# Performance work log

Measured on AMD Instinct MI355X. Metric: run time of the kernel, lower is better.

The kernel has to match this reference:

```python
import jax, jax.numpy as jnp
import numpy as np

E = 16        # num_experts
K = 2         # num_experts_per_tok
D = 1024      # dim
H = 2816      # moe_intermediate_size
S = 4096      # sequence_length (flattened tokens)


def setup_inputs() -> dict:
    key = jax.random.key(0)
    k0, k1, k2, k3, k4 = jax.random.split(key, 5)
    # gate: nn.Linear(dim, E) default init ~ U(-1/sqrt(D), 1/sqrt(D))
    gb = 1.0 / np.sqrt(D)
    gate_w = jax.random.uniform(k0, (E, D), minval=-gb, maxval=gb, dtype=jnp.float32)
    # MoeFusedLinear init: U(-sqrt(15/in), sqrt(15/in)), weight shape [E, out, in]
    b_d = np.sqrt(15.0 / D)
    b_h = np.sqrt(15.0 / H)
    w_gate = jax.random.uniform(k1, (E, H, D), minval=-b_d, maxval=b_d, dtype=jnp.float32)
    w_up = jax.random.uniform(k2, (E, H, D), minval=-b_d, maxval=b_d, dtype=jnp.float32)
    w_down = jax.random.uniform(k3, (E, D, H), minval=-b_h, maxval=b_h, dtype=jnp.float32)
    hidden_states = jax.random.normal(k4, (S, D), dtype=jnp.float32)
    return {"hidden_states": hidden_states, "gate_w": gate_w,
            "w_gate": w_gate, "w_up": w_up, "w_down": w_down}


def _grouped_mm(x_bf16, w, group_sizes):
    # emulate torch._grouped_mm: bf16 inputs, weight [E, out, in] -> rhs [E, in, out]
    rhs = jnp.swapaxes(w, 1, 2).astype(jnp.bfloat16)
    out = jax.lax.ragged_dot(x_bf16, rhs, group_sizes)
    return out.astype(jnp.float32)  # .to(input.dtype), input is fp32


def reference(hidden_states, gate_w, w_gate, w_up, w_down):
    # --- router (fp32) ---
    logits = hidden_states.astype(jnp.float32) @ gate_w.T              # [S, E]
    probs = jax.nn.softmax(logits, axis=-1)                            # fp32
    top_w, top_i = jax.lax.top_k(probs, K)                             # [S, K]
    rw = top_w / jnp.sum(top_w, axis=-1, keepdims=True)                # norm_topk_prob
    rw = rw.astype(hidden_states.dtype)
    # --- dispatch: replicate tokens K times, stable-sort by expert ---
    flat_e = top_i.reshape(-1)                                         # [S*K]
    sort_idx = jnp.argsort(flat_e, stable=True)
    inv_sort_idx = jnp.argsort(sort_idx)
    x_rep = jnp.repeat(hidden_states, K, axis=0)                       # [S*K, D]
    xs = x_rep[sort_idx].astype(jnp.bfloat16)
    group_sizes = jnp.bincount(flat_e, length=E).astype(jnp.int32)     # histc
    # --- grouped expert MLP (SwiGLU) ---
    g = _grouped_mm(xs, w_gate, group_sizes)                           # [S*K, H] fp32
    u = _grouped_mm(xs, w_up, group_sizes)
    h = (jax.nn.silu(g) * u).astype(jnp.bfloat16)
    y = _grouped_mm(h, w_down, group_sizes)                            # [S*K, D] fp32
    # --- combine ---
    y = y[inv_sort_idx].reshape(S, K, D)
    out = jnp.einsum('sko,sk->so', y, rw)                              # [S, D]
    return out, logits, top_i
```

## Files before the change

### kernel.cpp

```cpp
#include <hip/hip_runtime.h>

#define S_ 4096
#define E_ 16
#define K_ 2
#define D_ 1024
#define H_ 2816
#define MAXT 80
#define MP_ (MAXT * 128)

#define ME_CNT   0
#define ME_FILL  16
#define ME_POFF  32
#define ME_NT    48
#define ME_TE    64
#define ME_TR    (64 + MAXT)

#define WS_META   0
#define WS_SLOT   4096
#define WS_RW     36864
#define WS_TOPI   69632
#define WS_XS     (1u << 20)
#define WS_H      (WS_XS + (size_t)MP_ * D_ * 4)

typedef float floatx4 __attribute__((ext_vector_type(4)));
typedef __bf16 bf16x8 __attribute__((ext_vector_type(8)));

__device__ __forceinline__ unsigned short f2bf(float f) {
  unsigned u = __float_as_uint(f);
  u += 0x7fffu + ((u >> 16) & 1u);
  return (unsigned short)(u >> 16);
}
__device__ __forceinline__ unsigned pack2(float a, float b) {
  return (unsigned)f2bf(a) | ((unsigned)f2bf(b) << 16);
}

__global__ __launch_bounds__(256) void router_k(
    const float* __restrict__ x, const float* __restrict__ gw,
    float* __restrict__ logits_out, float* __restrict__ topi_out,
    float* __restrict__ rw, int* __restrict__ topi, int* __restrict__ meta)
{
  int s = blockIdx.x;
  int t = threadIdx.x;
  __shared__ float xl[D_];
  __shared__ float red[E_][16];
  __shared__ float lg[E_];
  for (int d = t; d < D_; d += 256) xl[d] = x[(size_t)s * D_ + d];
  __syncthreads();
  int e = t >> 4, i = t & 15;
  const float* g = gw + e * D_;
  float p = 0.f;
  for (int j = 0; j < 64; ++j) p += xl[i + 16 * j] * g[i + 16 * j];
  red[e][i] = p;
  __syncthreads();
  if (t < E_) {
    float sm = 0.f;
    for (int j = 0; j < 16; ++j) sm += red[t][j];
    lg[t] = sm;
    logits_out[(size_t)s * E_ + t] = sm;
  }
  __syncthreads();
  if (t == 0) {
    float mx = lg[0];
    for (int j = 1; j < E_; ++j) mx = fmaxf(mx, lg[j]);
    float pr[E_];
    for (int j = 0; j < E_; ++j) pr[j] = expf(lg[j] - mx);
    int i0 = 0; float b0 = pr[0];
    for (int j = 1; j < E_; ++j) if (pr[j] > b0) { b0 = pr[j]; i0 = j; }
    int i1 = -1; float b1 = -1.f;
    for (int j = 0; j < E_; ++j) if (j != i0 && pr[j] > b1) { b1 = pr[j]; i1 = j; }
    float w0 = b0 / (b0 + b1), w1 = b1 / (b0 + b1);
    topi_out[(size_t)s * K_ + 0] = (float)i0;
    topi_out[(size_t)s * K_ + 1] = (float)i1;
    rw[s * K_ + 0] = w0; rw[s * K_ + 1] = w1;
    topi[s * K_ + 0] = i0; topi[s * K_ + 1] = i1;
    atomicAdd(&meta[ME_CNT + i0], 1);
    atomicAdd(&meta[ME_CNT + i1], 1);
  }
}

__global__ void scan_k(int* __restrict__ meta) {
  if (threadIdx.x == 0 && blockIdx.x == 0) {
    int off = 0, nt = 0;
    for (int e = 0; e < E_; ++e) {
      meta[ME_POFF + e] = off;
      int c = meta[ME_CNT + e];
      int tiles = (c + 127) >> 7;
      for (int i = 0; i < tiles; ++i) { meta[ME_TE + nt] = e; meta[ME_TR + nt] = off + i * 128; ++nt; }
      off += tiles << 7;
    }
    meta[ME_NT] = nt;
  }
}

__global__ __launch_bounds__(256) void scatter_k(
    const int* __restrict__ topi, int* __restrict__ meta, int* __restrict__ slot_of)
{
  int idx = blockIdx.x * 256 + threadIdx.x;
  if (idx >= S_ * K_) return;
  int e = topi[idx];
  int pos = meta[ME_POFF + e] + atomicAdd(&meta[ME_FILL + e], 1);
  slot_of[idx] = pos;
}

__global__ __launch_bounds__(256) void gather_k(
    const float* __restrict__ x, const int* __restrict__ slot_of,
    unsigned short* __restrict__ xs)
{
  int idx = blockIdx.x;
  int s = idx >> 1;
  int pos = slot_of[idx];
  int t = threadIdx.x;
  float4 v = ((const float4*)(x + (size_t)s * D_))[t];
  ((uint2*)(xs + (size_t)pos * D_))[t] = make_uint2(pack2(v.x, v.y), pack2(v.z, v.w));
}

__global__ __launch_bounds__(256) void gemm1_k(
    const unsigned short* __restrict__ xs,
    const float* __restrict__ wg, const float* __restrict__ wu,
    unsigned short* __restrict__ h, const int* __restrict__ meta)
{
  int tile = blockIdx.x;
  if (tile >= meta[ME_NT]) return;
  int ntile = blockIdx.y;
  int e = meta[ME_TE + tile];
  int row0 = meta[ME_TR + tile];

  __shared__ uint4 As4[512];
  __shared__ uint4 Bg4[512];
  __shared__ uint4 Bu4[512];
  const unsigned short* As = (const unsigned short*)As4;
  const unsigned short* Bg = (const unsigned short*)Bg4;
  const unsigned short* Bu = (const unsigned short*)Bu4;

  int t = threadIdx.x;
  int lane = t & 63, w = t >> 6;
  int wm = w >> 1, wn = w & 1;

  const unsigned short* ap = xs + (size_t)row0 * D_;
  const float* wgp = wg + ((size_t)e * H_ + ntile * 128) * D_;
  const float* wup = wu + ((size_t)e * H_ + ntile * 128) * D_;

  floatx4 zero4 = {0.f, 0.f, 0.f, 0.f};
  floatx4 accg[4][4], accu[4][4];
  for (int a = 0; a < 4; ++a) for (int b = 0; b < 4; ++b) { accg[a][b] = zero4; accu[a][b] = zero4; }

  int bn = t >> 1, bkh = t & 1;

  for (int k0 = 0; k0 < D_; k0 += 32) {
    __syncthreads();
    {
      int c = t;
      As4[c] = *(const uint4*)(ap + (size_t)(c >> 2) * D_ + k0 + (c & 3) * 8);
      c = t + 256;
      As4[c] = *(const uint4*)(ap + (size_t)(c >> 2) * D_ + k0 + (c & 3) * 8);
    }
    {
      const float4* srcg = (const float4*)(wgp + (size_t)bn * D_ + k0 + bkh * 16);
      const float4* srcu = (const float4*)(wup + (size_t)bn * D_ + k0 + bkh * 16);
      float4 g0 = srcg[0], g1 = srcg[1], g2 = srcg[2], g3 = srcg[3];
      float4 u0 = srcu[0], u1 = srcu[1], u2 = srcu[2], u3 = srcu[3];
      int base = bn * 4 + bkh * 2;
      Bg4[base]     = make_uint4(pack2(g0.x, g0.y), pack2(g0.z, g0.w), pack2(g1.x, g1.y), pack2(g1.z, g1.w));
      Bg4[base + 1] = make_uint4(pack2(g2.x, g2.y), pack2(g2.z, g2.w), pack2(g3.x, g3.y), pack2(g3.z, g3.w));
      Bu4[base]     = make_uint4(pack2(u0.x, u0.y), pack2(u0.z, u0.w), pack2(u1.x, u1.y), pack2(u1.z, u1.w));
      Bu4[base + 1] = make_uint4(pack2(u2.x, u2.y), pack2(u2.z, u2.w), pack2(u3.x, u3.y), pack2(u3.z, u3.w));
    }
    __syncthreads();
    int mrow = lane & 15;
    int kq = (lane >> 4) * 8;
    bf16x8 af[4], bg[4], bu[4];
    for (int mi = 0; mi < 4; ++mi)
      af[mi] = *(const bf16x8*)(As + (wm * 64 + mi * 16 + mrow) * 32 + kq);
    for (int ni = 0; ni < 4; ++ni) {
      int r = (wn * 64 + ni * 16 + mrow) * 32 + kq;
      bg[ni] = *(const bf16x8*)(Bg + r);
      bu[ni] = *(const bf16x8*)(Bu + r);
    }
    for (int mi = 0; mi < 4; ++mi)
      for (int ni = 0; ni < 4; ++ni) {
        accg[mi][ni] = __builtin_amdgcn_mfma_f32_16x16x32_bf16(af[mi], bg[ni], accg[mi][ni], 0, 0, 0);
        accu[mi][ni] = __builtin_amdgcn_mfma_f32_16x16x32_bf16(af[mi], bu[ni], accu[mi][ni], 0, 0, 0);
      }
  }
  int colb = ntile * 128 + wn * 64;
  int rquad = (lane >> 4) * 4;
  for (int mi = 0; mi < 4; ++mi)
    for (int ni = 0; ni < 4; ++ni)
      for (int r = 0; r < 4; ++r) {
        int row = row0 + wm * 64 + mi * 16 + rquad + r;
        int col = colb + ni * 16 + (lane & 15);
        float gv = accg[mi][ni][r], uv = accu[mi][ni][r];
        float sv = gv / (1.f + expf(-gv));
        h[(size_t)row * H_ + col] = f2bf(sv * uv);
      }
}

__global__ __launch_bounds__(256) void gemm2_k(
    const unsigned short* __restrict__ hbuf,
    const float* __restrict__ wd,
    float* __restrict__ y, const int* __restrict__ meta)
{
  int tile = blockIdx.x;
  if (tile >= meta[ME_NT]) return;
  int ntile = blockIdx.y;
  int e = meta[ME_TE + tile];
  int row0 = meta[ME_TR + tile];

  __shared__ uint4 As4[512];
  __shared__ uint4 Bd4[512];
  const unsigned short* As = (const unsigned short*)As4;
  const unsigned short* Bd = (const unsigned short*)Bd4;

  int t = threadIdx.x;
  int lane = t & 63, w = t >> 6;
  int wm = w >> 1, wn = w & 1;

  const unsigned short* ap = hbuf + (size_t)row0 * H_;
  const float* wdp = wd + ((size_t)e * D_ + ntile * 128) * H_;

  floatx4 zero4 = {0.f, 0.f, 0.f, 0.f};
  floatx4 acc[4][4];
  for (int a = 0; a < 4; ++a) for (int b = 0; b < 4; ++b) acc[a][b] = zero4;

  int bn = t >> 1, bkh = t & 1;

  for (int k0 = 0; k0 < H_; k0 += 32) {
    __syncthreads();
    {
      int c = t;
      As4[c] = *(const uint4*)(ap + (size_t)(c >> 2) * H_ + k0 + (c & 3) * 8);
      c = t + 256;
      As4[c] = *(const uint4*)(ap + (size_t)(c >> 2) * H_ + k0 + (c & 3) * 8);
    }
    {
      const float4* srcd = (const float4*)(wdp + (size_t)bn * H_ + k0 + bkh * 16);
      float4 d0 = srcd[0], d1 = srcd[1], d2 = srcd[2], d3 = srcd[3];
      int base = bn * 4 + bkh * 2;
      Bd4[base]     = make_uint4(pack2(d0.x, d0.y), pack2(d0.z, d0.w), pack2(d1.x, d1.y), pack2(d1.z, d1.w));
      Bd4[base + 1] = make_uint4(pack2(d2.x, d2.y), pack2(d2.z, d2.w), pack2(d3.x, d3.y), pack2(d3.z, d3.w));
    }
    __syncthreads();
    int mrow = lane & 15;
    int kq = (lane >> 4) * 8;
    bf16x8 af[4], bf[4];
    for (int mi = 0; mi < 4; ++mi)
      af[mi] = *(const bf16x8*)(As + (wm * 64 + mi * 16 + mrow) * 32 + kq);
    for (int ni = 0; ni < 4; ++ni)
      bf[ni] = *(const bf16x8*)(Bd + (wn * 64 + ni * 16 + mrow) * 32 + kq);
    for (int mi = 0; mi < 4; ++mi)
      for (int ni = 0; ni < 4; ++ni)
        acc[mi][ni] = __builtin_amdgcn_mfma_f32_16x16x32_bf16(af[mi], bf[ni], acc[mi][ni], 0, 0, 0);
  }
  int colb = ntile * 128 + wn * 64;
  int rquad = (lane >> 4) * 4;
  for (int mi = 0; mi < 4; ++mi)
    for (int ni = 0; ni < 4; ++ni)
      for (int r = 0; r < 4; ++r) {
        int row = row0 + wm * 64 + mi * 16 + rquad + r;
        int col = colb + ni * 16 + (lane & 15);
        y[(size_t)row * D_ + col] = acc[mi][ni][r];
      }
}

__global__ __launch_bounds__(256) void combine_k(
    const float* __restrict__ y, const float* __restrict__ rw,
    const int* __restrict__ slot_of, float* __restrict__ out)
{
  int s = blockIdx.x, t = threadIdx.x;
  int s0 = slot_of[s * 2], s1 = slot_of[s * 2 + 1];
  float w0 = rw[s * 2], w1 = rw[s * 2 + 1];
  float4 a = ((const float4*)(y + (size_t)s0 * D_))[t];
  float4 b = ((const float4*)(y + (size_t)s1 * D_))[t];
  float4 o;
  o.x = w0 * a.x + w1 * b.x;
  o.y = w0 * a.y + w1 * b.y;
  o.z = w0 * a.z + w1 * b.z;
  o.w = w0 * a.w + w1 * b.w;
  ((float4*)(out + (size_t)s * D_))[t] = o;
}

extern "C" void kernel_launch(void* const* d_in, const int* in_sizes, int n_in,
                              void* d_out, int out_size, void* d_ws, size_t ws_size,
                              hipStream_t stream) {
  const float* x  = (const float*)d_in[0];
  const float* gw = (const float*)d_in[1];
  const float* wg = (const float*)d_in[2];
  const float* wu = (const float*)d_in[3];
  const float* wd = (const float*)d_in[4];

  float* out = (float*)d_out;
  float* logits_out = out + (size_t)S_ * D_;
  float* topi_out = logits_out + (size_t)S_ * E_;

  char* ws = (char*)d_ws;
  int* meta = (int*)(ws + WS_META);
  int* slot_of = (int*)(ws + WS_SLOT);
  float* rw = (float*)(ws + WS_RW);
  int* topi = (int*)(ws + WS_TOPI);
  unsigned short* xs = (unsigned short*)(ws + WS_XS);
  float* y = (float*)(ws + WS_XS);
  unsigned short* h = (unsigned short*)(ws + WS_H);

  hipMemsetAsync(meta, 0, 4096, stream);
  hipMemsetAsync(xs, 0, (size_t)MP_ * D_ * 2, stream);

  router_k<<<S_, 256, 0, stream>>>(x, gw, logits_out, topi_out, rw, topi, meta);
  scan_k<<<1, 64, 0, stream>>>(meta);
  scatter_k<<<(S_ * K_ + 255) / 256, 256, 0, stream>>>(topi, meta, slot_of);
  gather_k<<<S_ * K_, 256, 0, stream>>>(x, slot_of, xs);
  gemm1_k<<<dim3(MAXT, H_ / 128), 256, 0, stream>>>(xs, wg, wu, h, meta);
  gemm2_k<<<dim3(MAXT, D_ / 128), 256, 0, stream>>>(h, wd, y, meta);
  combine_k<<<S_, 256, 0, stream>>>(y, rw, slot_of, out);
}
```

Measured before the change: 1.177 ms.

## Pre-convert expert weights to bf16 and use direct global-to-LDS loads in GEMMs

Adds kernels that convert the fp32 gate/up/down weights to bf16 once per call, interleaving gate and up rows so a single GEMM produces both and the SwiGLU pairs them through a lane shuffle. The new GEMMs stage A and B tiles with global_load_lds and a 64-wide K step, so the inner loop no longer converts fp32 weights. This avoids redundant fp32 weight reads and conversion across the 80 row tiles, at the cost of an extra full weight pass and a large workspace. It falls back to the old path when the workspace is too small.

```diff
diff --git a/kernel.cpp b/kernel.cpp
--- a/kernel.cpp
+++ b/kernel.cpp
@@ -5,6 +5,7 @@
 #define K_ 2
 #define D_ 1024
 #define H_ 2816
+#define H2_ (2 * H_)
 #define MAXT 80
 #define MP_ (MAXT * 128)
 
@@ -21,6 +22,8 @@
 #define WS_TOPI   69632
 #define WS_XS     (1u << 20)
 #define WS_H      (WS_XS + (size_t)MP_ * D_ * 4)
+#define WS_W      (WS_H + (size_t)MP_ * H_ * 2)
+#define WS_NEED   (WS_W + (size_t)E_ * H2_ * D_ * 2)
 
 typedef float floatx4 __attribute__((ext_vector_type(4)));
 typedef __bf16 bf16x8 __attribute__((ext_vector_type(8)));
@@ -32,6 +35,11 @@
 }
 __device__ __forceinline__ unsigned pack2(float a, float b) {
   return (unsigned)f2bf(a) | ((unsigned)f2bf(b) << 16);
+}
+__device__ __forceinline__ void gl_lds16(const unsigned short* g, unsigned short* l) {
+  __builtin_amdgcn_global_load_lds(
+      (const __attribute__((address_space(1))) unsigned int*)g,
+      (__attribute__((address_space(3))) unsigned int*)l, 16, 0, 0);
 }
 
 __global__ __launch_bounds__(256) void router_k(
@@ -114,9 +122,34 @@
   ((uint2*)(xs + (size_t)pos * D_))[t] = make_uint2(pack2(v.x, v.y), pack2(v.z, v.w));
 }
 
-__global__ __launch_bounds__(256) void gemm1_k(
-    const unsigned short* __restrict__ xs,
+__global__ __launch_bounds__(128) void convert_gu_k(
     const float* __restrict__ wg, const float* __restrict__ wu,
+    unsigned short* __restrict__ W1)
+{
+  int r = blockIdx.x;
+  int e = blockIdx.y;
+  int j = r >> 1;
+  const float* src = ((r & 1) ? wu : wg) + ((size_t)e * H_ + j) * D_;
+  unsigned short* dst = W1 + ((size_t)e * H2_ + r) * D_;
+  int t = threadIdx.x;
+  float4 a = ((const float4*)src)[2 * t];
+  float4 b = ((const float4*)src)[2 * t + 1];
+  ((uint4*)dst)[t] = make_uint4(pack2(a.x, a.y), pack2(a.z, a.w),
+                                pack2(b.x, b.y), pack2(b.z, b.w));
+}
+
+__global__ __launch_bounds__(256) void convert_d_k(
+    const float* __restrict__ wd, unsigned short* __restrict__ W2)
+{
+  size_t i = (size_t)blockIdx.x * 256 + threadIdx.x;
+  float4 a = ((const float4*)wd)[2 * i];
+  float4 b = ((const float4*)wd)[2 * i + 1];
+  ((uint4*)W2)[i] = make_uint4(pack2(a.x, a.y), pack2(a.z, a.w),
+                               pack2(b.x, b.y), pack2(b.z, b.w));
+}
+
+__global__ __launch_bounds__(256) void gemm1_f(
+    const unsigned short* __restrict__ xs, const unsigned short* __restrict__ W1,
     unsigned short* __restrict__ h, const int* __restrict__ meta)
 {
   int tile = blockIdx.x;
@@ -125,27 +158,166 @@
   int e = meta[ME_TE + tile];
   int row0 = meta[ME_TR + tile];
 
+  __shared__ unsigned short As[128 * 64];
+  __shared__ unsigned short Bs[128 * 64];
+
+  int t = threadIdx.x, lane = t & 63, w = t >> 6;
+  int wm = w >> 1, wn = w & 1;
+
+  const unsigned short* ap = xs + ((size_t)row0 + w * 32 + (lane >> 3)) * D_ + (lane & 7) * 8;
+  const unsigned short* bp = W1 + ((size_t)e * H2_ + ntile * 128 + w * 32 + (lane >> 3)) * D_ + (lane & 7) * 8;
+  unsigned short* la = As + (w * 32) * 64;
+  unsigned short* lb = Bs + (w * 32) * 64;
+
+  floatx4 acc[4][4];
+  floatx4 zero4 = {0.f, 0.f, 0.f, 0.f};
+#pragma unroll
+  for (int a = 0; a < 4; ++a)
+#pragma unroll
+    for (int b = 0; b < 4; ++b) acc[a][b] = zero4;
+
+  int mrow = lane & 15, kq = (lane >> 4) * 8;
+
+  for (int k0 = 0; k0 < D_; k0 += 64) {
+    __syncthreads();
+#pragma unroll
+    for (int i = 0; i < 4; ++i) {
+      gl_lds16(ap + k0 + i * 8 * D_, la + i * 8 * 64);
+      gl_lds16(bp + k0 + i * 8 * D_, lb + i * 8 * 64);
+    }
+    __syncthreads();
+#pragma unroll
+    for (int kk = 0; kk < 64; kk += 32) {
+      bf16x8 af[4], bfv[4];
+#pragma unroll
+      for (int mi = 0; mi < 4; ++mi)
+        af[mi] = *(const bf16x8*)(As + (wm * 64 + mi * 16 + mrow) * 64 + kk + kq);
+#pragma unroll
+      for (int ni = 0; ni < 4; ++ni)
+        bfv[ni] = *(const bf16x8*)(Bs + (wn * 64 + ni * 16 + mrow) * 64 + kk + kq);
+#pragma unroll
+      for (int mi = 0; mi < 4; ++mi)
+#pragma unroll
+        for (int ni = 0; ni < 4; ++ni)
+          acc[mi][ni] = __builtin_amdgcn_mfma_f32_16x16x32_bf16(af[mi], bfv[ni], acc[mi][ni], 0, 0, 0);
+    }
+  }
+
+  int rquad = (lane >> 4) * 4;
+  int colb = ntile * 128 + wn * 64;
+#pragma unroll
+  for (int mi = 0; mi < 4; ++mi)
+#pragma unroll
+    for (int ni = 0; ni < 4; ++ni)
+#pragma unroll
+      for (int r = 0; r < 4; ++r) {
+        float v = acc[mi][ni][r];
+        float p = __shfl_xor(v, 1, 64);
+        int col = colb + ni * 16 + (lane & 15);
+        float gv = (col & 1) ? p : v;
+        float uv = (col & 1) ? v : p;
+        float hv = gv / (1.f + expf(-gv)) * uv;
+        if (!(col & 1)) {
+          int row = row0 + wm * 64 + mi * 16 + rquad + r;
+          h[(size_t)row * H_ + (col >> 1)] = f2bf(hv);
+        }
+      }
+}
+
+__global__ __launch_bounds__(256) void gemm2_f(
+    const unsigned short* __restrict__ hbuf, const unsigned short* __restrict__ W2,
+    float* __restrict__ y, const int* __restrict__ meta)
+{
+  int tile = blockIdx.x;
+  if (tile >= meta[ME_NT]) return;
+  int ntile = blockIdx.y;
+  int e = meta[ME_TE + tile];
+  int row0 = meta[ME_TR + tile];
+
+  __shared__ unsigned short As[128 * 64];
+  __shared__ unsigned short Bs[128 * 64];
+
+  int t = threadIdx.x, lane = t & 63, w = t >> 6;
+  int wm = w >> 1, wn = w & 1;
+
+  const unsigned short* ap = hbuf + ((size_t)row0 + w * 32 + (lane >> 3)) * H_ + (lane & 7) * 8;
+  const unsigned short* bp = W2 + ((size_t)e * D_ + ntile * 128 + w * 32 + (lane >> 3)) * H_ + (lane & 7) * 8;
+  unsigned short* la = As + (w * 32) * 64;
+  unsigned short* lb = Bs + (w * 32) * 64;
+
+  floatx4 acc[4][4];
+  floatx4 zero4 = {0.f, 0.f, 0.f, 0.f};
+#pragma unroll
+  for (int a = 0; a < 4; ++a)
+#pragma unroll
+    for (int b = 0; b < 4; ++b) acc[a][b] = zero4;
+
+  int mrow = lane & 15, kq = (lane >> 4) * 8;
+
+  for (int k0 = 0; k0 < H_; k0 += 64) {
+    __syncthreads();
+#pragma unroll
+    for (int i = 0; i < 4; ++i) {
+      gl_lds16(ap + k0 + i * 8 * H_, la + i * 8 * 64);
+      gl_lds16(bp + k0 + i * 8 * H_, lb + i * 8 * 64);
+    }
+    __syncthreads();
+#pragma unroll
+    for (int kk = 0; kk < 64; kk += 32) {
+      bf16x8 af[4], bfv[4];
+#pragma unroll
+      for (int mi = 0; mi < 4; ++mi)
+        af[mi] = *(const bf16x8*)(As + (wm * 64 + mi * 16 + mrow) * 64 + kk + kq);
+#pragma unroll
+      for (int ni = 0; ni < 4; ++ni)
+        bfv[ni] = *(const bf16x8*)(Bs + (wn * 64 + ni * 16 + mrow) * 64 + kk + kq);
+#pragma unroll
+      for (int mi = 0; mi < 4; ++mi)
+#pragma unroll
+        for (int ni = 0; ni < 4; ++ni)
+          acc[mi][ni] = __builtin_amdgcn_mfma_f32_16x16x32_bf16(af[mi], bfv[ni], acc[mi][ni], 0, 0, 0);
+    }
+  }
+
+  int rquad = (lane >> 4) * 4;
+  int colb = ntile * 128 + wn * 64;
+#pragma unroll
+  for (int mi = 0; mi < 4; ++mi)
+#pragma unroll
+    for (int ni = 0; ni < 4; ++ni)
+#pragma unroll
+      for (int r = 0; r < 4; ++r) {
+        int row = row0 + wm * 64 + mi * 16 + rquad + r;
+        y[(size_t)row * D_ + colb + ni * 16 + (lane & 15)] = acc[mi][ni][r];
+      }
+}
+
+__global__ __launch_bounds__(256) void gemm1_k(
+    const unsigned short* __restrict__ xs,
+    const float* __restrict__ wg, const float* __restrict__ wu,
+    unsigned short* __restrict__ h, const int* __restrict__ meta)
+{
+  int tile = blockIdx.x;
+  if (tile >= meta[ME_NT]) return;
+  int ntile = blockIdx.y;
+  int e = meta[ME_TE + tile];
+  int row0 = meta[ME_TR + tile];
   __shared__ uint4 As4[512];
   __shared__ uint4 Bg4[512];
   __shared__ uint4 Bu4[512];
   const unsigned short* As = (const unsigned short*)As4;
   const unsigned short* Bg = (const unsigned short*)Bg4;
   const unsigned short* Bu = (const unsigned short*)Bu4;
-
   int t = threadIdx.x;
   int lane = t & 63, w = t >> 6;
   int wm = w >> 1, wn = w & 1;
-
   const unsigned short* ap = xs + (size_t)row0 * D_;
   const float* wgp = wg + ((size_t)e * H_ + ntile * 128) * D_;
   const float* wup = wu + ((size_t)e * H_ + ntile * 128) * D_;
-
   floatx4 zero4 = {0.f, 0.f, 0.f, 0.f};
   floatx4 accg[4][4], accu[4][4];
   for (int a = 0; a < 4; ++a) for (int b = 0; b < 4; ++b) { accg[a][b] = zero4; accu[a][b] = zero4; }
-
   int bn = t >> 1, bkh = t & 1;
-
   for (int k0 = 0; k0 < D_; k0 += 32) {
     __syncthreads();
     {
@@ -205,25 +377,19 @@
   int ntile = blockIdx.y;
   int e = meta[ME_TE + tile];
   int row0 = meta[ME_TR + tile];
-
   __shared__ uint4 As4[512];
   __shared__ uint4 Bd4[512];
   const unsigned short* As = (const unsigned short*)As4;
   const unsigned short* Bd = (const unsigned short*)Bd4;
-
   int t = threadIdx.x;
   int lane = t & 63, w = t >> 6;
   int wm = w >> 1, wn = w & 1;
-
   const unsigned short* ap = hbuf + (size_t)row0 * H_;
   const float* wdp = wd + ((size_t)e * D_ + ntile * 128) * H_;
-
   floatx4 zero4 = {0.f, 0.f, 0.f, 0.f};
   floatx4 acc[4][4];
   for (int a = 0; a < 4; ++a) for (int b = 0; b < 4; ++b) acc[a][b] = zero4;
-
   int bn = t >> 1, bkh = t & 1;
-
   for (int k0 = 0; k0 < H_; k0 += 32) {
     __syncthreads();
     {
@@ -242,14 +408,14 @@
     __syncthreads();
     int mrow = lane & 15;
     int kq = (lane >> 4) * 8;
-    bf16x8 af[4], bf[4];
+    bf16x8 af[4], bfv[4];
     for (int mi = 0; mi < 4; ++mi)
       af[mi] = *(const bf16x8*)(As + (wm * 64 + mi * 16 + mrow) * 32 + kq);
     for (int ni = 0; ni < 4; ++ni)
-      bf[ni] = *(const bf16x8*)(Bd + (wn * 64 + ni * 16 + mrow) * 32 + kq);
+      bfv[ni] = *(const bf16x8*)(Bd + (wn * 64 + ni * 16 + mrow) * 32 + kq);
     for (int mi = 0; mi < 4; ++mi)
       for (int ni = 0; ni < 4; ++ni)
-        acc[mi][ni] = __builtin_amdgcn_mfma_f32_16x16x32_bf16(af[mi], bf[ni], acc[mi][ni], 0, 0, 0);
+        acc[mi][ni] = __builtin_amdgcn_mfma_f32_16x16x32_bf16(af[mi], bfv[ni], acc[mi][ni], 0, 0, 0);
   }
   int colb = ntile * 128 + wn * 64;
   int rquad = (lane >> 4) * 4;
@@ -300,6 +466,8 @@
   unsigned short* xs = (unsigned short*)(ws + WS_XS);
   float* y = (float*)(ws + WS_XS);
   unsigned short* h = (unsigned short*)(ws + WS_H);
+  unsigned short* W1 = (unsigned short*)(ws + WS_W);
+  unsigned short* W2 = W1;
 
   hipMemsetAsync(meta, 0, 4096, stream);
   hipMemsetAsync(xs, 0, (size_t)MP_ * D_ * 2, stream);
@@ -308,7 +476,15 @@
   scan_k<<<1, 64, 0, stream>>>(meta);
   scatter_k<<<(S_ * K_ + 255) / 256, 256, 0, stream>>>(topi, meta, slot_of);
   gather_k<<<S_ * K_, 256, 0, stream>>>(x, slot_of, xs);
-  gemm1_k<<<dim3(MAXT, H_ / 128), 256, 0, stream>>>(xs, wg, wu, h, meta);
-  gemm2_k<<<dim3(MAXT, D_ / 128), 256, 0, stream>>>(h, wd, y, meta);
+
+  if (ws_size >= WS_NEED) {
+    convert_gu_k<<<dim3(H2_, E_), 128, 0, stream>>>(wg, wu, W1);
+    gemm1_f<<<dim3(MAXT, H2_ / 128), 256, 0, stream>>>(xs, W1, h, meta);
+    convert_d_k<<<(E_ * D_ * H_ / 8) / 256, 256, 0, stream>>>(wd, W2);
+    gemm2_f<<<dim3(MAXT, D_ / 128), 256, 0, stream>>>(h, W2, y, meta);
+  } else {
+    gemm1_k<<<dim3(MAXT, H_ / 128), 256, 0, stream>>>(xs, wg, wu, h, meta);
+    gemm2_k<<<dim3(MAXT, D_ / 128), 256, 0, stream>>>(h, wd, y, meta);
+  }
   combine_k<<<S_, 256, 0, stream>>>(y, rw, slot_of, out);
 }
```

New measurement: 1.020 ms. 1.15x faster.
